# Kernel optimization log

Measured on AMD Instinct MI355X. Metric: run time of the kernel, lower is better.

The kernel has to match this reference:

```python
import jax, jax.numpy as jnp
import numpy as np

K_CURV = 1.0   # Lorentz(k=1.0)
EPS = 1e-6


def _project(space):
    # lift space components onto hyperboloid: t = sqrt(k + ||s||^2)
    t = jnp.sqrt(K_CURV + jnp.sum(space * space, axis=-1, keepdims=True))
    return jnp.concatenate([t, space], axis=-1)


def setup_inputs():
    key = jax.random.key(0)
    B, N, D, H = 4, 1024, 128, 8
    ks = jax.random.split(key, 7)
    # valid Lorentz points: [B, N, D] with x[...,0] the time coordinate
    x = _project(jax.random.normal(ks[0], (B, N, D - 1), dtype=jnp.float32) * 0.5)
    scale = 1.0 / np.sqrt(D)
    Wq = jax.random.normal(ks[1], (H, D - 1, D), dtype=jnp.float32) * scale
    Wk = jax.random.normal(ks[2], (H, D - 1, D), dtype=jnp.float32) * scale
    Wv = jax.random.normal(ks[3], (H, D - 1, D), dtype=jnp.float32) * scale
    bq = jnp.zeros((H, D - 1), dtype=jnp.float32)
    bk = jnp.zeros((H, D - 1), dtype=jnp.float32)
    bv = jnp.zeros((H, D - 1), dtype=jnp.float32)
    beta = jnp.ones((H,), dtype=jnp.float32)
    gamma = jnp.zeros((H,), dtype=jnp.float32)
    return {"x": x, "Wq": Wq, "bq": bq, "Wk": Wk, "bk": bk, "Wv": Wv, "bv": bv,
            "beta": beta, "gamma": gamma}


def _lorentz_fc(x, W, b):
    # HyboNet-style Lorentz fully-connected (identity activation), all heads at once.
    # x: [B,N,D], W: [H,D-1,D], b: [H,D-1] -> [H,B,N,D] on the hyperboloid
    space = jnp.einsum('bnd,hed->hbne', x, W) + b[:, None, None, :]
    return _project(space)


def reference(x, Wq, bq, Wk, bk, Wv, bv, beta, gamma):
    D = x.shape[-1]
    sign = jnp.concatenate([-jnp.ones((1,), x.dtype), jnp.ones((D - 1,), x.dtype)])
    Q = _lorentz_fc(x, Wq, bq)   # [H,B,N,D]
    K = _lorentz_fc(x, Wk, bk)
    V = _lorentz_fc(x, Wv, bv)
    # pairwise Minkowski inner product <q,k>_L = -t_q t_k + s_q . s_k
    inner = jnp.einsum('hbid,hbjd->hbij', Q * sign, K)          # [H,B,N,N]
    dists = jnp.arccosh(jnp.maximum(-inner / K_CURV, 1.0 + EPS)) * np.sqrt(K_CURV)
    scores = -beta[:, None, None, None] * dists - gamma[:, None, None, None]
    attn = jax.nn.softmax(scores, axis=-1)
    # Lorentz midpoint: normalize weighted sum back onto the hyperboloid
    mid = jnp.einsum('hbij,hbjd->hbid', attn, V)                # [H,B,N,D]
    mnorm = jnp.einsum('hbid,hbid->hbi', mid * sign, mid)       # <m,m>_L (negative)
    head_out = mid * (np.sqrt(K_CURV) / jnp.sqrt(jnp.maximum(-mnorm, EPS)))[..., None]
    # direct_concat: concatenate space parts, recompute time coordinate
    H = head_out.shape[0]
    t = head_out[..., 0]                                        # [H,B,N]
    s = jnp.moveaxis(head_out[..., 1:], 0, 2)                   # [B,N,H,D-1]
    space_cat = s.reshape(s.shape[0], s.shape[1], -1)           # [B,N,H*(D-1)]
    time = jnp.sqrt(jnp.maximum(jnp.sum(t * t, axis=0) - (H - 1) * K_CURV, EPS))
    return jnp.concatenate([time[..., None], space_cat], axis=-1)  # [B,N,H*(D-1)+1]
```

## Files before the change

kernel.cpp:

```cpp
#include <hip/hip_runtime.h>

typedef __attribute__((ext_vector_type(8))) short short8_t;
typedef __attribute__((ext_vector_type(4))) short short4_t;
typedef __attribute__((ext_vector_type(4))) float float4_t;
typedef __attribute__((ext_vector_type(2))) unsigned int uint2_t;

__device__ __forceinline__ unsigned short f2bf(float f) {
    unsigned u = __builtin_bit_cast(unsigned, f);
    u += 0x7FFFu + ((u >> 16) & 1u);
    return (unsigned short)(u >> 16);
}

__device__ __forceinline__ unsigned pk_bf16(float a, float b) {
    unsigned r;
    asm("v_cvt_pk_bf16_f32 %0, %1, %2" : "=v"(r) : "v"(a), "v"(b));
    return r;
}

#define MFMA(A, B, C) __builtin_amdgcn_mfma_f32_16x16x32_bf16((A), (B), (C), 0, 0, 0)

__global__ __launch_bounds__(256, 2) void k_proj(
    const float* __restrict__ x,
    const float* __restrict__ Wq, const float* __restrict__ bq,
    const float* __restrict__ Wk, const float* __restrict__ bk,
    const float* __restrict__ Wv, const float* __restrict__ bv,
    unsigned short* __restrict__ Qs, unsigned short* __restrict__ Kb,
    unsigned short* __restrict__ Vt)
{
    __shared__ __align__(16) unsigned char lds[71680];
    unsigned short* Xs  = (unsigned short*)lds;
    unsigned short* Ws  = (unsigned short*)(lds + 17408);
    unsigned short* Ot  = (unsigned short*)(lds + 52224);
    float*          ssqB = (float*)(lds + 70656);

    const int tid = threadIdx.x;
    const int m0  = blockIdx.x * 64;
    const int h   = blockIdx.y;

    #pragma unroll
    for (int p = 0; p < 8; p++) {
        int r = p * 8 + (tid >> 5), c = (tid & 31) * 4;
        float4_t v = *(const float4_t*)(x + (m0 + r) * 128 + c);
        uint2_t u; u[0] = pk_bf16(v[0], v[1]); u[1] = pk_bf16(v[2], v[3]);
        *(uint2_t*)(Xs + r * 136 + c) = u;
    }
    const int we = tid >> 5, wc = (tid & 31) * 4;
    float4_t wreg[16];
    #pragma unroll
    for (int p = 0; p < 16; p++) {
        int e = p * 8 + we;
        wreg[p] = (e < 127) ? *(const float4_t*)(Wq + (h * 127 + e) * 128 + wc)
                            : (float4_t){0.f, 0.f, 0.f, 0.f};
    }

    const int w = tid >> 6, lane = tid & 63, li = lane & 15, lg = lane >> 4;

    for (int mat = 0; mat < 3; mat++) {
        #pragma unroll
        for (int p = 0; p < 16; p++) {
            int e = p * 8 + we;
            uint2_t u; u[0] = pk_bf16(wreg[p][0], wreg[p][1]);
                       u[1] = pk_bf16(wreg[p][2], wreg[p][3]);
            *(uint2_t*)(Ws + e * 136 + wc) = u;
        }
        if (mat < 2) {
            const float* Wn = (mat == 0) ? Wk : Wv;
            #pragma unroll
            for (int p = 0; p < 16; p++) {
                int e = p * 8 + we;
                wreg[p] = (e < 127) ? *(const float4_t*)(Wn + (h * 127 + e) * 128 + wc)
                                    : (float4_t){0.f, 0.f, 0.f, 0.f};
            }
        }
        __syncthreads();

        float4_t acc[4][2];
        #pragma unroll
        for (int i = 0; i < 4; i++)
            #pragma unroll
            for (int j = 0; j < 2; j++) acc[i][j] = (float4_t){0.f, 0.f, 0.f, 0.f};

        #pragma unroll
        for (int kk = 0; kk < 4; kk++) {
            short8_t Bf[2];
            #pragma unroll
            for (int ni = 0; ni < 2; ni++)
                Bf[ni] = *(short8_t*)(Ws + (w * 32 + ni * 16 + li) * 136 + kk * 32 + lg * 8);
            #pragma unroll
            for (int mi = 0; mi < 4; mi++) {
                short8_t A = *(short8_t*)(Xs + (mi * 16 + li) * 136 + kk * 32 + lg * 8);
                #pragma unroll
                for (int ni = 0; ni < 2; ni++) acc[mi][ni] = MFMA(A, Bf[ni], acc[mi][ni]);
            }
        }
        const float* bb = (mat == 0) ? bq : ((mat == 1) ? bk : bv);
        #pragma unroll
        for (int ni = 0; ni < 2; ni++) {
            int e = w * 32 + ni * 16 + li;
            float bvv = (e < 127) ? bb[h * 127 + e] : 0.0f;
            #pragma unroll
            for (int mi = 0; mi < 4; mi++)
                #pragma unroll
                for (int r = 0; r < 4; r++) acc[mi][ni][r] += bvv;
        }
        #pragma unroll
        for (int mi = 0; mi < 4; mi++) {
            #pragma unroll
            for (int r = 0; r < 4; r++) {
                float s = acc[mi][0][r] * acc[mi][0][r] + acc[mi][1][r] * acc[mi][1][r];
                s += __shfl_xor(s, 1);  s += __shfl_xor(s, 2);
                s += __shfl_xor(s, 4);  s += __shfl_xor(s, 8);
                if (li == 0) ssqB[(mi * 16 + lg * 4 + r) * 4 + w] = s;
            }
        }
        __syncthreads();

        if (mat < 2) {
            #pragma unroll
            for (int mi = 0; mi < 4; mi++)
                #pragma unroll
                for (int ni = 0; ni < 2; ni++) {
                    int e = w * 32 + ni * 16 + li;
                    if (e < 127) {
                        #pragma unroll
                        for (int r = 0; r < 4; r++)
                            Ot[(mi * 16 + lg * 4 + r) * 136 + 1 + e] = f2bf(acc[mi][ni][r]);
                    }
                }
            if (tid < 64) {
                float s = ssqB[tid * 4] + ssqB[tid * 4 + 1] + ssqB[tid * 4 + 2] + ssqB[tid * 4 + 3];
                float t = sqrtf(1.0f + s);
                Ot[tid * 136] = f2bf(mat == 0 ? -t : t);
            }
            __syncthreads();
            unsigned short* dst = ((mat == 0) ? Qs : Kb) + (h * 4096 + m0) * 128;
            #pragma unroll
            for (int p = 0; p < 4; p++) {
                int r = p * 16 + (tid >> 4), c = (tid & 15) * 8;
                *(short8_t*)(dst + r * 128 + c) = *(short8_t*)(Ot + r * 136 + c);
            }
        } else {
            #pragma unroll
            for (int mi = 0; mi < 4; mi++)
                #pragma unroll
                for (int ni = 0; ni < 2; ni++) {
                    int e = w * 32 + ni * 16 + li;
                    if (e < 127) {
                        uint2_t u;
                        u[0] = pk_bf16(acc[mi][ni][0], acc[mi][ni][1]);
                        u[1] = pk_bf16(acc[mi][ni][2], acc[mi][ni][3]);
                        *(uint2_t*)(Ot + (1 + e) * 72 + mi * 16 + lg * 4) = u;
                    }
                }
            if (tid < 64) {
                float s = ssqB[tid * 4] + ssqB[tid * 4 + 1] + ssqB[tid * 4 + 2] + ssqB[tid * 4 + 3];
                Ot[tid] = f2bf(sqrtf(1.0f + s));
            }
            __syncthreads();
            int b = m0 >> 10, n0 = m0 & 1023;
            unsigned short* dst = Vt + (h * 4 + b) * 131072 + n0;
            #pragma unroll
            for (int p = 0; p < 4; p++) {
                int d = p * 32 + (tid >> 3), nc = (tid & 7) * 8;
                *(short8_t*)(dst + d * 1024 + nc) = *(short8_t*)(Ot + d * 72 + nc);
            }
        }
    }
}

__global__ __launch_bounds__(256) void k_attn(
    const unsigned short* __restrict__ Qsg, const unsigned short* __restrict__ Kb,
    const unsigned short* __restrict__ Vt,
    const float* __restrict__ beta, const float* __restrict__ gamma,
    float* __restrict__ out, float* __restrict__ tsq)
{
    __shared__ __align__(16) unsigned char lds[80896];
    unsigned short* Kbuf0 = (unsigned short*)lds;
    unsigned short* Kbuf1 = (unsigned short*)(lds + 17408);
    unsigned short* Vbuf0 = (unsigned short*)(lds + 34816);
    unsigned short* Vbuf1 = (unsigned short*)(lds + 53248);
    unsigned short* Ps    = (unsigned short*)(lds + 71680);
    float*          ow    = (float*)lds;

    const int tid = threadIdx.x, w = tid >> 6, lane = tid & 63;
    const int li = lane & 15, lg = lane >> 4;

    const int bid = blockIdx.x;
    const int hb = (bid & 7) * 4 + (bid >> 7);
    const int qt = (bid >> 3) & 15;
    const int h = hb >> 2, b = hb & 3;
    const int q0 = qt * 64;

    const unsigned short* Qp = Qsg + (h * 4096 + b * 1024) * 128;
    const unsigned short* Kp = Kb  + (h * 4096 + b * 1024) * 128;
    const unsigned short* Vp = Vt  + (h * 4 + b) * 131072;
    const float bet = beta[h];
    (void)gamma;

    const int kr = tid >> 4, kc = (tid & 15) * 8;
    const int vd = tid >> 3, vc = (tid & 7) * 8;
    const unsigned short* Kld = Kp + kr * 128 + kc;
    const unsigned short* Vld = Vp + vd * 1024 + vc;

    short8_t qf[4];
    const int qrow = q0 + w * 16 + li;
    #pragma unroll
    for (int kk = 0; kk < 4; kk++)
        qf[kk] = *(const short8_t*)(Qp + qrow * 128 + kk * 32 + lg * 8);

    float4_t amid[8];
    #pragma unroll
    for (int df = 0; df < 8; df++) amid[df] = (float4_t){0.f, 0.f, 0.f, 0.f};
    float m = -INFINITY, lsum = 0.0f;

    short8_t kreg[4], vreg[4];
    #pragma unroll
    for (int p = 0; p < 4; p++) {
        kreg[p] = *(const short8_t*)(Kld + p * 2048);
        vreg[p] = *(const short8_t*)(Vld + p * 32768);
    }
    #pragma unroll
    for (int p = 0; p < 4; p++) {
        *(short8_t*)(Kbuf0 + (p * 16 + kr) * 136 + kc) = kreg[p];
        *(short8_t*)(Vbuf0 + (p * 32 + vd) * 72 + vc) = vreg[p];
    }
    __syncthreads();

    for (int t = 0; t < 16; t++) {
        unsigned short* Kc = (t & 1) ? Kbuf1 : Kbuf0;
        unsigned short* Vc = (t & 1) ? Vbuf1 : Vbuf0;
        unsigned short* Kn = (t & 1) ? Kbuf0 : Kbuf1;
        unsigned short* Vn = (t & 1) ? Vbuf0 : Vbuf1;

        if (t < 15) {
            const int j0n = (t + 1) * 64;
            #pragma unroll
            for (int p = 0; p < 4; p++) {
                kreg[p] = *(const short8_t*)(Kld + j0n * 128 + p * 2048);
                vreg[p] = *(const short8_t*)(Vld + p * 32768 + j0n);
            }
        }
        __builtin_amdgcn_sched_barrier(0);

        float4_t as[4];
        #pragma unroll
        for (int jf = 0; jf < 4; jf++) as[jf] = (float4_t){0.f, 0.f, 0.f, 0.f};
        __builtin_amdgcn_s_setprio(1);
        #pragma unroll
        for (int kk = 0; kk < 4; kk++) {
            #pragma unroll
            for (int jf = 0; jf < 4; jf++) {
                short8_t A = *(short8_t*)(Kc + (jf * 16 + li) * 136 + kk * 32 + lg * 8);
                as[jf] = MFMA(A, qf[kk], as[jf]);
            }
        }
        __builtin_amdgcn_s_setprio(0);

        float s2[16];
        float tm = -INFINITY;
        #pragma unroll
        for (int jf = 0; jf < 4; jf++) {
            #pragma unroll
            for (int r = 0; r < 4; r++) {
                float z = fmaxf(-as[jf][r], 1.0f + 1e-6f);
                float wv = z + __builtin_amdgcn_sqrtf(__builtin_fmaf(z, z, -1.0f));
                float s = -bet * __builtin_amdgcn_logf(wv);
                s2[jf * 4 + r] = s;
                tm = fmaxf(tm, s);
            }
        }
        tm = fmaxf(tm, __shfl_xor(tm, 16));
        tm = fmaxf(tm, __shfl_xor(tm, 32));
        if (__any(tm > m + 8.0f)) {
            float mn = fmaxf(m, tm);
            float scale = __builtin_amdgcn_exp2f(m - mn);
            lsum *= scale;
            #pragma unroll
            for (int df = 0; df < 8; df++)
                #pragma unroll
                for (int r = 0; r < 4; r++) amid[df][r] *= scale;
            m = mn;
        }
        float ps_ = 0.0f;
        #pragma unroll
        for (int jf = 0; jf < 4; jf++) {
            float p0 = __builtin_amdgcn_exp2f(s2[jf * 4 + 0] - m);
            float p1 = __builtin_amdgcn_exp2f(s2[jf * 4 + 1] - m);
            float p2 = __builtin_amdgcn_exp2f(s2[jf * 4 + 2] - m);
            float p3 = __builtin_amdgcn_exp2f(s2[jf * 4 + 3] - m);
            ps_ += (p0 + p1) + (p2 + p3);
            uint2_t u; u[0] = pk_bf16(p0, p1); u[1] = pk_bf16(p2, p3);
            *(uint2_t*)(Ps + (w * 16 + li) * 72 + jf * 16 + lg * 4) = u;
        }
        ps_ += __shfl_xor(ps_, 16);
        ps_ += __shfl_xor(ps_, 32);
        lsum += ps_;
        asm volatile("s_waitcnt lgkmcnt(0)" ::: "memory");
        __builtin_amdgcn_sched_barrier(0);

        __builtin_amdgcn_s_setprio(1);
        #pragma unroll
        for (int kk2 = 0; kk2 < 2; kk2++) {
            short8_t Bp = *(short8_t*)(Ps + (w * 16 + li) * 72 + kk2 * 32 + lg * 8);
            #pragma unroll
            for (int df = 0; df < 8; df++) {
                short8_t A = *(short8_t*)(Vc + (df * 16 + li) * 72 + kk2 * 32 + lg * 8);
                amid[df] = MFMA(A, Bp, amid[df]);
            }
        }
        __builtin_amdgcn_s_setprio(0);

        if (t < 15) {
            #pragma unroll
            for (int p = 0; p < 4; p++) {
                *(short8_t*)(Kn + (p * 16 + kr) * 136 + kc) = kreg[p];
                *(short8_t*)(Vn + (p * 32 + vd) * 72 + vc) = vreg[p];
            }
        }
        __syncthreads();
    }

    float invl = 1.0f / lsum;
    float ssq = 0.0f;
    #pragma unroll
    for (int df = 0; df < 8; df++) {
        #pragma unroll
        for (int r = 0; r < 4; r++) {
            float v = amid[df][r] * invl;
            amid[df][r] = v;
            ssq += v * v;
        }
    }
    ssq += __shfl_xor(ssq, 16);
    ssq += __shfl_xor(ssq, 32);
    float tmid = __shfl(amid[0][0], li);
    float denom = fmaxf(2.0f * tmid * tmid - ssq, 1e-6f);
    float rs = 1.0f / sqrtf(denom);

    #pragma unroll
    for (int df = 0; df < 8; df++) {
        #pragma unroll
        for (int r = 0; r < 4; r++)
            ow[w * 2112 + li * 132 + df * 16 + lg * 4 + r] = amid[df][r] * rs;
    }
    asm volatile("s_waitcnt lgkmcnt(0)" ::: "memory");
    __builtin_amdgcn_sched_barrier(0);

    #pragma unroll
    for (int i = 0; i < 16; i++) {
        int n = q0 + w * 16 + i;
        float v0 = ow[w * 2112 + i * 132 + lane];
        float v1 = ow[w * 2112 + i * 132 + 64 + lane];
        float* orow = out + (b * 1024 + n) * 1017;
        if (lane == 0) tsq[h * 4096 + b * 1024 + n] = v0 * v0;
        else           orow[h * 127 + lane] = v0;
        orow[h * 127 + 64 + lane] = v1;
    }
}

__global__ __launch_bounds__(256) void k_time(const float* __restrict__ tsq,
                                              float* __restrict__ out)
{
    int mrow = blockIdx.x * 256 + threadIdx.x;
    float s = 0.0f;
    #pragma unroll
    for (int h = 0; h < 8; h++) s += tsq[h * 4096 + mrow];
    out[mrow * 1017] = sqrtf(fmaxf(s - 7.0f, 1e-6f));
}

extern "C" void kernel_launch(void* const* d_in, const int* in_sizes, int n_in,
                              void* d_out, int out_size, void* d_ws, size_t ws_size,
                              hipStream_t stream)
{
    const float* x    = (const float*)d_in[0];
    const float* Wq   = (const float*)d_in[1];
    const float* bq   = (const float*)d_in[2];
    const float* Wk   = (const float*)d_in[3];
    const float* bk   = (const float*)d_in[4];
    const float* Wv   = (const float*)d_in[5];
    const float* bv   = (const float*)d_in[6];
    const float* beta = (const float*)d_in[7];
    const float* gam  = (const float*)d_in[8];
    float* out = (float*)d_out;

    unsigned char* ws = (unsigned char*)d_ws;
    unsigned short* Qs = (unsigned short*)(ws);
    unsigned short* Kb = (unsigned short*)(ws + 8388608);
    unsigned short* Vt = (unsigned short*)(ws + 16777216);
    float*          ts = (float*)(ws + 25165824);

    k_proj<<<dim3(64, 8), 256, 0, stream>>>(x, Wq, bq, Wk, bk, Wv, bv, Qs, Kb, Vt);
    k_attn<<<dim3(512), 256, 0, stream>>>(Qs, Kb, Vt, beta, gam, out, ts);
    k_time<<<dim3(16), 256, 0, stream>>>(ts, out);
}
```

Measured before the change: 143.7 us.

## Split projection over Q/K/V grid dimension and add beta==1 softmax fast path

The projection kernel now launches one block per (tile, head, matrix) instead of looping over Q, K and V inside a block. This triples the grid, reuses the weight buffer as the output staging area to cut LDS use, and drops the register prefetch of the next weight matrix. The attention kernel gains a fast path for beta==1: exp(-arccosh(z)) becomes 1/(z+sqrt(z^2-1)), which removes log, exp and running-max rescaling. It also gets launch_bounds occupancy hint 2. The fast path depends on beta being exactly 1 and assumes a fixed max of 0, which is numerically fine because scores are at most 0.

```diff
diff --git a/kernel.cpp b/kernel.cpp
--- a/kernel.cpp
+++ b/kernel.cpp
@@ -19,7 +19,7 @@
 
 #define MFMA(A, B, C) __builtin_amdgcn_mfma_f32_16x16x32_bf16((A), (B), (C), 0, 0, 0)
 
-__global__ __launch_bounds__(256, 2) void k_proj(
+__global__ __launch_bounds__(256) void k_proj(
     const float* __restrict__ x,
     const float* __restrict__ Wq, const float* __restrict__ bq,
     const float* __restrict__ Wk, const float* __restrict__ bk,
@@ -27,15 +27,19 @@
     unsigned short* __restrict__ Qs, unsigned short* __restrict__ Kb,
     unsigned short* __restrict__ Vt)
 {
-    __shared__ __align__(16) unsigned char lds[71680];
+    __shared__ __align__(16) unsigned char lds[17408 + 34816 + 1024];
     unsigned short* Xs  = (unsigned short*)lds;
     unsigned short* Ws  = (unsigned short*)(lds + 17408);
-    unsigned short* Ot  = (unsigned short*)(lds + 52224);
-    float*          ssqB = (float*)(lds + 70656);
+    float*          ssqB = (float*)(lds + 17408 + 34816);
+    unsigned short* Ot  = Ws;
+    unsigned short* OtT = Ws;
 
     const int tid = threadIdx.x;
     const int m0  = blockIdx.x * 64;
     const int h   = blockIdx.y;
+    const int mat = blockIdx.z;
+    const float* W  = (mat == 0) ? Wq : ((mat == 1) ? Wk : Wv);
+    const float* bb = (mat == 0) ? bq : ((mat == 1) ? bk : bv);
 
     #pragma unroll
     for (int p = 0; p < 8; p++) {
@@ -44,131 +48,110 @@
         uint2_t u; u[0] = pk_bf16(v[0], v[1]); u[1] = pk_bf16(v[2], v[3]);
         *(uint2_t*)(Xs + r * 136 + c) = u;
     }
-    const int we = tid >> 5, wc = (tid & 31) * 4;
-    float4_t wreg[16];
     #pragma unroll
     for (int p = 0; p < 16; p++) {
-        int e = p * 8 + we;
-        wreg[p] = (e < 127) ? *(const float4_t*)(Wq + (h * 127 + e) * 128 + wc)
-                            : (float4_t){0.f, 0.f, 0.f, 0.f};
-    }
+        int e = p * 8 + (tid >> 5), c = (tid & 31) * 4;
+        float4_t v = {0.f, 0.f, 0.f, 0.f};
+        if (e < 127) v = *(const float4_t*)(W + (h * 127 + e) * 128 + c);
+        uint2_t u; u[0] = pk_bf16(v[0], v[1]); u[1] = pk_bf16(v[2], v[3]);
+        *(uint2_t*)(Ws + e * 136 + c) = u;
+    }
+    __syncthreads();
 
     const int w = tid >> 6, lane = tid & 63, li = lane & 15, lg = lane >> 4;
-
-    for (int mat = 0; mat < 3; mat++) {
-        #pragma unroll
-        for (int p = 0; p < 16; p++) {
-            int e = p * 8 + we;
-            uint2_t u; u[0] = pk_bf16(wreg[p][0], wreg[p][1]);
-                       u[1] = pk_bf16(wreg[p][2], wreg[p][3]);
-            *(uint2_t*)(Ws + e * 136 + wc) = u;
-        }
-        if (mat < 2) {
-            const float* Wn = (mat == 0) ? Wk : Wv;
-            #pragma unroll
-            for (int p = 0; p < 16; p++) {
-                int e = p * 8 + we;
-                wreg[p] = (e < 127) ? *(const float4_t*)(Wn + (h * 127 + e) * 128 + wc)
-                                    : (float4_t){0.f, 0.f, 0.f, 0.f};
-            }
+    float4_t acc[4][2];
+    #pragma unroll
+    for (int i = 0; i < 4; i++)
+        #pragma unroll
+        for (int j = 0; j < 2; j++) acc[i][j] = (float4_t){0.f, 0.f, 0.f, 0.f};
+
+    #pragma unroll
+    for (int kk = 0; kk < 4; kk++) {
+        short8_t Bf[2];
+        #pragma unroll
+        for (int ni = 0; ni < 2; ni++)
+            Bf[ni] = *(short8_t*)(Ws + (w * 32 + ni * 16 + li) * 136 + kk * 32 + lg * 8);
+        #pragma unroll
+        for (int mi = 0; mi < 4; mi++) {
+            short8_t A = *(short8_t*)(Xs + (mi * 16 + li) * 136 + kk * 32 + lg * 8);
+            #pragma unroll
+            for (int ni = 0; ni < 2; ni++) acc[mi][ni] = MFMA(A, Bf[ni], acc[mi][ni]);
+        }
+    }
+    #pragma unroll
+    for (int ni = 0; ni < 2; ni++) {
+        int e = w * 32 + ni * 16 + li;
+        float bvv = (e < 127) ? bb[h * 127 + e] : 0.0f;
+        #pragma unroll
+        for (int mi = 0; mi < 4; mi++)
+            #pragma unroll
+            for (int r = 0; r < 4; r++) acc[mi][ni][r] += bvv;
+    }
+    #pragma unroll
+    for (int mi = 0; mi < 4; mi++) {
+        #pragma unroll
+        for (int r = 0; r < 4; r++) {
+            float s = acc[mi][0][r] * acc[mi][0][r] + acc[mi][1][r] * acc[mi][1][r];
+            s += __shfl_xor(s, 1);  s += __shfl_xor(s, 2);
+            s += __shfl_xor(s, 4);  s += __shfl_xor(s, 8);
+            if (li == 0) ssqB[(mi * 16 + lg * 4 + r) * 4 + w] = s;
+        }
+    }
+    __syncthreads();
+
+    if (mat < 2) {
+        #pragma unroll
+        for (int mi = 0; mi < 4; mi++)
+            #pragma unroll
+            for (int ni = 0; ni < 2; ni++) {
+                int e = w * 32 + ni * 16 + li;
+                if (e < 127) {
+                    #pragma unroll
+                    for (int r = 0; r < 4; r++)
+                        Ot[(mi * 16 + lg * 4 + r) * 136 + 1 + e] = f2bf(acc[mi][ni][r]);
+                }
+            }
+        if (tid < 64) {
+            float s = ssqB[tid * 4] + ssqB[tid * 4 + 1] + ssqB[tid * 4 + 2] + ssqB[tid * 4 + 3];
+            float t = sqrtf(1.0f + s);
+            Ot[tid * 136] = f2bf(mat == 0 ? -t : t);
         }
         __syncthreads();
-
-        float4_t acc[4][2];
-        #pragma unroll
-        for (int i = 0; i < 4; i++)
-            #pragma unroll
-            for (int j = 0; j < 2; j++) acc[i][j] = (float4_t){0.f, 0.f, 0.f, 0.f};
-
-        #pragma unroll
-        for (int kk = 0; kk < 4; kk++) {
-            short8_t Bf[2];
-            #pragma unroll
-            for (int ni = 0; ni < 2; ni++)
-                Bf[ni] = *(short8_t*)(Ws + (w * 32 + ni * 16 + li) * 136 + kk * 32 + lg * 8);
-            #pragma unroll
-            for (int mi = 0; mi < 4; mi++) {
-                short8_t A = *(short8_t*)(Xs + (mi * 16 + li) * 136 + kk * 32 + lg * 8);
-                #pragma unroll
-                for (int ni = 0; ni < 2; ni++) acc[mi][ni] = MFMA(A, Bf[ni], acc[mi][ni]);
-            }
-        }
-        const float* bb = (mat == 0) ? bq : ((mat == 1) ? bk : bv);
-        #pragma unroll
-        for (int ni = 0; ni < 2; ni++) {
-            int e = w * 32 + ni * 16 + li;
-            float bvv = (e < 127) ? bb[h * 127 + e] : 0.0f;
-            #pragma unroll
-            for (int mi = 0; mi < 4; mi++)
-                #pragma unroll
-                for (int r = 0; r < 4; r++) acc[mi][ni][r] += bvv;
-        }
-        #pragma unroll
-        for (int mi = 0; mi < 4; mi++) {
-            #pragma unroll
-            for (int r = 0; r < 4; r++) {
-                float s = acc[mi][0][r] * acc[mi][0][r] + acc[mi][1][r] * acc[mi][1][r];
-                s += __shfl_xor(s, 1);  s += __shfl_xor(s, 2);
-                s += __shfl_xor(s, 4);  s += __shfl_xor(s, 8);
-                if (li == 0) ssqB[(mi * 16 + lg * 4 + r) * 4 + w] = s;
-            }
+        unsigned short* dst = ((mat == 0) ? Qs : Kb) + (h * 4096 + m0) * 128;
+        #pragma unroll
+        for (int p = 0; p < 4; p++) {
+            int r = p * 16 + (tid >> 4), c = (tid & 15) * 8;
+            *(short8_t*)(dst + r * 128 + c) = *(short8_t*)(Ot + r * 136 + c);
+        }
+    } else {
+        #pragma unroll
+        for (int mi = 0; mi < 4; mi++)
+            #pragma unroll
+            for (int ni = 0; ni < 2; ni++) {
+                int e = w * 32 + ni * 16 + li;
+                if (e < 127) {
+                    uint2_t u;
+                    u[0] = pk_bf16(acc[mi][ni][0], acc[mi][ni][1]);
+                    u[1] = pk_bf16(acc[mi][ni][2], acc[mi][ni][3]);
+                    *(uint2_t*)(OtT + (1 + e) * 72 + mi * 16 + lg * 4) = u;
+                }
+            }
+        if (tid < 64) {
+            float s = ssqB[tid * 4] + ssqB[tid * 4 + 1] + ssqB[tid * 4 + 2] + ssqB[tid * 4 + 3];
+            OtT[tid] = f2bf(sqrtf(1.0f + s));
         }
         __syncthreads();
-
-        if (mat < 2) {
-            #pragma unroll
-            for (int mi = 0; mi < 4; mi++)
-                #pragma unroll
-                for (int ni = 0; ni < 2; ni++) {
-                    int e = w * 32 + ni * 16 + li;
-                    if (e < 127) {
-                        #pragma unroll
-                        for (int r = 0; r < 4; r++)
-                            Ot[(mi * 16 + lg * 4 + r) * 136 + 1 + e] = f2bf(acc[mi][ni][r]);
-                    }
-                }
-            if (tid < 64) {
-                float s = ssqB[tid * 4] + ssqB[tid * 4 + 1] + ssqB[tid * 4 + 2] + ssqB[tid * 4 + 3];
-                float t = sqrtf(1.0f + s);
-                Ot[tid * 136] = f2bf(mat == 0 ? -t : t);
-            }
-            __syncthreads();
-            unsigned short* dst = ((mat == 0) ? Qs : Kb) + (h * 4096 + m0) * 128;
-            #pragma unroll
-            for (int p = 0; p < 4; p++) {
-                int r = p * 16 + (tid >> 4), c = (tid & 15) * 8;
-                *(short8_t*)(dst + r * 128 + c) = *(short8_t*)(Ot + r * 136 + c);
-            }
-        } else {
-            #pragma unroll
-            for (int mi = 0; mi < 4; mi++)
-                #pragma unroll
-                for (int ni = 0; ni < 2; ni++) {
-                    int e = w * 32 + ni * 16 + li;
-                    if (e < 127) {
-                        uint2_t u;
-                        u[0] = pk_bf16(acc[mi][ni][0], acc[mi][ni][1]);
-                        u[1] = pk_bf16(acc[mi][ni][2], acc[mi][ni][3]);
-                        *(uint2_t*)(Ot + (1 + e) * 72 + mi * 16 + lg * 4) = u;
-                    }
-                }
-            if (tid < 64) {
-                float s = ssqB[tid * 4] + ssqB[tid * 4 + 1] + ssqB[tid * 4 + 2] + ssqB[tid * 4 + 3];
-                Ot[tid] = f2bf(sqrtf(1.0f + s));
-            }
-            __syncthreads();
-            int b = m0 >> 10, n0 = m0 & 1023;
-            unsigned short* dst = Vt + (h * 4 + b) * 131072 + n0;
-            #pragma unroll
-            for (int p = 0; p < 4; p++) {
-                int d = p * 32 + (tid >> 3), nc = (tid & 7) * 8;
-                *(short8_t*)(dst + d * 1024 + nc) = *(short8_t*)(Ot + d * 72 + nc);
-            }
-        }
-    }
-}
-
-__global__ __launch_bounds__(256) void k_attn(
+        int b = m0 >> 10, n0 = m0 & 1023;
+        unsigned short* dst = Vt + (h * 4 + b) * 131072 + n0;
+        #pragma unroll
+        for (int p = 0; p < 4; p++) {
+            int d = p * 32 + (tid >> 3), nc = (tid & 7) * 8;
+            *(short8_t*)(dst + d * 1024 + nc) = *(short8_t*)(OtT + d * 72 + nc);
+        }
+    }
+}
+
+__global__ __launch_bounds__(256, 2) void k_attn(
     const unsigned short* __restrict__ Qsg, const unsigned short* __restrict__ Kb,
     const unsigned short* __restrict__ Vt,
     const float* __restrict__ beta, const float* __restrict__ gamma,
@@ -195,6 +178,7 @@
     const unsigned short* Kp = Kb  + (h * 4096 + b * 1024) * 128;
     const unsigned short* Vp = Vt  + (h * 4 + b) * 131072;
     const float bet = beta[h];
+    const bool beta1 = (bet == 1.0f);
     (void)gamma;
 
     const int kr = tid >> 4, kc = (tid & 15) * 8;
@@ -256,41 +240,57 @@
         }
         __builtin_amdgcn_s_setprio(0);
 
-        float s2[16];
-        float tm = -INFINITY;
-        #pragma unroll
-        for (int jf = 0; jf < 4; jf++) {
-            #pragma unroll
-            for (int r = 0; r < 4; r++) {
-                float z = fmaxf(-as[jf][r], 1.0f + 1e-6f);
-                float wv = z + __builtin_amdgcn_sqrtf(__builtin_fmaf(z, z, -1.0f));
-                float s = -bet * __builtin_amdgcn_logf(wv);
-                s2[jf * 4 + r] = s;
-                tm = fmaxf(tm, s);
-            }
-        }
-        tm = fmaxf(tm, __shfl_xor(tm, 16));
-        tm = fmaxf(tm, __shfl_xor(tm, 32));
-        if (__any(tm > m + 8.0f)) {
-            float mn = fmaxf(m, tm);
-            float scale = __builtin_amdgcn_exp2f(m - mn);
-            lsum *= scale;
-            #pragma unroll
-            for (int df = 0; df < 8; df++)
+        float ps_ = 0.0f;
+        if (beta1) {
+            #pragma unroll
+            for (int jf = 0; jf < 4; jf++) {
+                float p[4];
                 #pragma unroll
-                for (int r = 0; r < 4; r++) amid[df][r] *= scale;
-            m = mn;
-        }
-        float ps_ = 0.0f;
-        #pragma unroll
-        for (int jf = 0; jf < 4; jf++) {
-            float p0 = __builtin_amdgcn_exp2f(s2[jf * 4 + 0] - m);
-            float p1 = __builtin_amdgcn_exp2f(s2[jf * 4 + 1] - m);
-            float p2 = __builtin_amdgcn_exp2f(s2[jf * 4 + 2] - m);
-            float p3 = __builtin_amdgcn_exp2f(s2[jf * 4 + 3] - m);
-            ps_ += (p0 + p1) + (p2 + p3);
-            uint2_t u; u[0] = pk_bf16(p0, p1); u[1] = pk_bf16(p2, p3);
-            *(uint2_t*)(Ps + (w * 16 + li) * 72 + jf * 16 + lg * 4) = u;
+                for (int r = 0; r < 4; r++) {
+                    float z = fmaxf(-as[jf][r], 1.0f + 1e-6f);
+                    float wv = z + __builtin_amdgcn_sqrtf(__builtin_fmaf(z, z, -1.0f));
+                    p[r] = __builtin_amdgcn_rcpf(wv);
+                    ps_ += p[r];
+                }
+                uint2_t u; u[0] = pk_bf16(p[0], p[1]); u[1] = pk_bf16(p[2], p[3]);
+                *(uint2_t*)(Ps + (w * 16 + li) * 72 + jf * 16 + lg * 4) = u;
+            }
+        } else {
+            float s2[16];
+            float tm = -INFINITY;
+            #pragma unroll
+            for (int jf = 0; jf < 4; jf++) {
+                #pragma unroll
+                for (int r = 0; r < 4; r++) {
+                    float z = fmaxf(-as[jf][r], 1.0f + 1e-6f);
+                    float wv = z + __builtin_amdgcn_sqrtf(__builtin_fmaf(z, z, -1.0f));
+                    float s = -bet * __builtin_amdgcn_logf(wv);
+                    s2[jf * 4 + r] = s;
+                    tm = fmaxf(tm, s);
+                }
+            }
+            tm = fmaxf(tm, __shfl_xor(tm, 16));
+            tm = fmaxf(tm, __shfl_xor(tm, 32));
+            if (__any(tm > m + 8.0f)) {
+                float mn = fmaxf(m, tm);
+                float scale = __builtin_amdgcn_exp2f(m - mn);
+                lsum *= scale;
+                #pragma unroll
+                for (int df = 0; df < 8; df++)
+                    #pragma unroll
+                    for (int r = 0; r < 4; r++) amid[df][r] *= scale;
+                m = mn;
+            }
+            #pragma unroll
+            for (int jf = 0; jf < 4; jf++) {
+                float p0 = __builtin_amdgcn_exp2f(s2[jf * 4 + 0] - m);
+                float p1 = __builtin_amdgcn_exp2f(s2[jf * 4 + 1] - m);
+                float p2 = __builtin_amdgcn_exp2f(s2[jf * 4 + 2] - m);
+                float p3 = __builtin_amdgcn_exp2f(s2[jf * 4 + 3] - m);
+                ps_ += (p0 + p1) + (p2 + p3);
+                uint2_t u; u[0] = pk_bf16(p0, p1); u[1] = pk_bf16(p2, p3);
+                *(uint2_t*)(Ps + (w * 16 + li) * 72 + jf * 16 + lg * 4) = u;
+            }
         }
         ps_ += __shfl_xor(ps_, 16);
         ps_ += __shfl_xor(ps_, 32);
@@ -389,7 +389,7 @@
     unsigned short* Vt = (unsigned short*)(ws + 16777216);
     float*          ts = (float*)(ws + 25165824);
 
-    k_proj<<<dim3(64, 8), 256, 0, stream>>>(x, Wq, bq, Wk, bk, Wv, bv, Qs, Kb, Vt);
+    k_proj<<<dim3(64, 8, 3), 256, 0, stream>>>(x, Wq, bq, Wk, bk, Wv, bv, Qs, Kb, Vt);
     k_attn<<<dim3(512), 256, 0, stream>>>(Qs, Kb, Vt, beta, gam, out, ts);
     k_time<<<dim3(16), 256, 0, stream>>>(ts, out);
 }
```

Result: faster. 136.7 us (-4.9%).
